# Performance work log

Hardware: AMD Instinct MI355X
Metric: run time of the kernel (lower is better)

## Reference

```python
import jax, jax.numpy as jnp
import numpy as np

B, W, E, P, H, NH = 2, 512, 2, 8, 1024, 16
D = H // NH  # 64
T = W + E


def _split_heads(x):
    # [..., S, H] -> [..., NH, S, D]
    x = x.reshape(x.shape[:-1] + (NH, D))
    return jnp.swapaxes(x, -2, -3)


def setup_inputs() -> dict:
    key = jax.random.key(0)
    ks = jax.random.split(key, 16)
    s = 0.02
    inp = {
        "word_hidden_states": jax.random.normal(ks[0], (B, W, H), jnp.float32),
        "entity_hidden_states": jax.random.normal(ks[1], (B, P, E, H), jnp.float32),
        "attention_mask": jnp.zeros((B, 1, 1, T), jnp.float32),
        "q_w": jax.random.normal(ks[2], (H, H), jnp.float32) * s,
        "q_b": jnp.zeros((H,), jnp.float32),
        "k_w": jax.random.normal(ks[3], (H, H), jnp.float32) * s,
        "k_b": jnp.zeros((H,), jnp.float32),
        "v_w": jax.random.normal(ks[4], (H, H), jnp.float32) * s,
        "v_b": jnp.zeros((H,), jnp.float32),
        "w2e_w": jax.random.normal(ks[5], (H, H), jnp.float32) * s,
        "w2e_b": jnp.zeros((H,), jnp.float32),
        "e2w_w": jax.random.normal(ks[6], (H, H), jnp.float32) * s,
        "e2w_b": jnp.zeros((H,), jnp.float32),
        "e2e_w": jax.random.normal(ks[7], (H, H), jnp.float32) * s,
        "e2e_b": jnp.zeros((H,), jnp.float32),
    }
    return inp


def reference(word_hidden_states, entity_hidden_states, attention_mask,
              q_w, q_b, k_w, k_b, v_w, v_b,
              w2e_w, w2e_b, e2w_w, e2w_b, e2e_w, e2e_b):
    words = word_hidden_states          # [B, W, H]
    ents = entity_hidden_states         # [B, P, E, H]

    # Queries: words use `query` and `w2e_query`; entities use `e2w_query` and `e2e_query`.
    w2w_q = _split_heads(words @ q_w + q_b)      # [B, NH, W, D]
    w2e_q = _split_heads(words @ w2e_w + w2e_b)  # [B, NH, W, D]
    e2w_q = _split_heads(ents @ e2w_w + e2w_b)   # [B, P, NH, E, D]
    e2e_q = _split_heads(ents @ e2e_w + e2e_b)   # [B, P, NH, E, D]

    # Shared key/value projection on [expanded words ; entities]. Word K/V are
    # identical across pairs (expand), so compute once and broadcast.
    k_word = _split_heads(words @ k_w + k_b)     # [B, NH, W, D]
    k_ent = _split_heads(ents @ k_w + k_b)       # [B, P, NH, E, D]
    v_word = _split_heads(words @ v_w + v_b)     # [B, NH, W, D]
    v_ent = _split_heads(ents @ v_w + v_b)       # [B, P, NH, E, D]

    # Four block score matrices.
    s_w2w = jnp.einsum('bhqd,bhkd->bhqk', w2w_q, k_word)      # [B, NH, W, W]
    s_w2e = jnp.einsum('bhqd,bphkd->bphqk', w2e_q, k_ent)     # [B, P, NH, W, E]
    s_e2w = jnp.einsum('bphqd,bhkd->bphqk', e2w_q, k_word)    # [B, P, NH, E, W]
    s_e2e = jnp.einsum('bphqd,bphkd->bphqk', e2e_q, k_ent)    # [B, P, NH, E, E]

    word_scores = jnp.concatenate(
        [jnp.broadcast_to(s_w2w[:, None], (B, P, NH, W, W)), s_w2e], axis=-1)
    ent_scores = jnp.concatenate([s_e2w, s_e2e], axis=-1)
    scores = jnp.concatenate([word_scores, ent_scores], axis=-2)  # [B, P, NH, T, T]

    scale = jnp.asarray(1.0 / np.sqrt(D), scores.dtype)
    scores = scores * scale + attention_mask[:, None]  # mask broadcasts [B,1,1,1,T]
    probs = jax.nn.softmax(scores, axis=-1)  # dropout: eval mode (deterministic)

    v = jnp.concatenate(
        [jnp.broadcast_to(v_word[:, None], (B, P, NH, W, D)), v_ent], axis=-2)
    ctx = jnp.einsum('bphqk,bphkd->bphqd', probs, v)   # [B, P, NH, T, D]
    ctx = jnp.swapaxes(ctx, -2, -3).reshape(B, P, T, H)

    word_reps = ctx[:, :, :W, :]   # [B, P, W, H]
    ent_reps = ctx[:, :, W:, :]    # [B, P, E, H]
    return (word_reps, ent_reps)
```

## Files before the change

kernel.cpp:

```cpp
#include <hip/hip_runtime.h>
#include <hip/hip_bf16.h>

typedef __attribute__((ext_vector_type(8))) short s16x8;
typedef __attribute__((ext_vector_type(4))) float fx4;
typedef __attribute__((ext_vector_type(4))) unsigned int u32x4;
typedef unsigned short u16;
typedef unsigned int   u32;
typedef unsigned long long u64;

#define DI __device__ __forceinline__


DI float bf2f(u16 x){ u32 u = ((u32)x)<<16; float f; __builtin_memcpy(&f,&u,4); return f; }
DI u16 f2bf(float f){ u32 u; __builtin_memcpy(&u,&f,4); u = (u + 0x7fffu + ((u>>16)&1u))>>16; return (u16)u; }

DI fx4 mfma_16x16x32_bf16(s16x8 a, s16x8 b, fx4 c){
  return __builtin_amdgcn_mfma_f32_16x16x32_bf16(a,b,c,0,0,0);
}

__global__ __launch_bounds__(256) void k_prep(
    const float* __restrict__ s0, const float* __restrict__ s1, const float* __restrict__ s2,
    const float* __restrict__ s3, const float* __restrict__ s4, const float* __restrict__ s5,
    u16* __restrict__ dstbase,
    const float* __restrict__ words, u16* __restrict__ Xbf,
    const float* __restrict__ ents,  u16* __restrict__ Ebf)
{
  __shared__ __align__(16) u16 tile[64][72];
  int bx = blockIdx.x, tid = threadIdx.x;
  if(bx < 1536){
    int z = bx>>8, t = bx&255;
    const float* src = (z==0)?s0:(z==1)?s1:(z==2)?s2:(z==3)?s3:(z==4)?s4:s5;
    u16* dst = dstbase + (u64)z*1048576u;
    int kt = (t&15)*64, nt = (t>>4)*64;
    #pragma unroll
    for(int it=0; it<2; ++it){
      int c = it*256 + tid;
      int r = c>>3, col = (c&7)*8;
      const float* sp = src + (u64)(kt+r)*1024u + nt + col;
      fx4 a = *(const fx4*)sp;
      fx4 b = *(const fx4*)(sp+4);
      u16 o[8];
      o[0]=f2bf(a[0]); o[1]=f2bf(a[1]); o[2]=f2bf(a[2]); o[3]=f2bf(a[3]);
      o[4]=f2bf(b[0]); o[5]=f2bf(b[1]); o[6]=f2bf(b[2]); o[7]=f2bf(b[3]);
      __builtin_memcpy(&tile[r][col], o, 16);
    }
    __syncthreads();
    #pragma unroll
    for(int it=0; it<2; ++it){
      int c = it*256 + tid;
      int nr = c>>3, kc = (c&7)*8;
      u16 tmp[8];
      #pragma unroll
      for(int j=0;j<8;++j) tmp[j] = tile[kc+j][nr];
      u32x4 v; __builtin_memcpy(&v, tmp, 16);
      *(u32x4*)(dst + (u64)(nt+nr)*1024u + kt + kc) = v;
    }
  } else {
    const float* src; u16* dst; int i;
    if(bx < 2048){ src = words; dst = Xbf; i = ((bx-1536)*256 + tid)*8; }
    else         { src = ents;  dst = Ebf; i = ((bx-2048)*256 + tid)*8; }
    fx4 a = *(const fx4*)(src+i);
    fx4 b = *(const fx4*)(src+i+4);
    u16 o[8];
    o[0]=f2bf(a[0]); o[1]=f2bf(a[1]); o[2]=f2bf(a[2]); o[3]=f2bf(a[3]);
    o[4]=f2bf(b[0]); o[5]=f2bf(b[1]); o[6]=f2bf(b[2]); o[7]=f2bf(b[3]);
    u32x4 v; __builtin_memcpy(&v,o,16);
    *(u32x4*)(dst+i)=v;
  }
}

__global__ __launch_bounds__(256) void k_proj(
    const u16* __restrict__ Xbf, const u16* __restrict__ Ebf,
    const u16* __restrict__ wtq, const u16* __restrict__ wtw2e,
    const u16* __restrict__ wtk, const u16* __restrict__ wtv,
    const u16* __restrict__ wte2w, const u16* __restrict__ wte2e,
    const float* __restrict__ qb, const float* __restrict__ w2eb,
    const float* __restrict__ kb, const float* __restrict__ vb,
    const float* __restrict__ e2wb, const float* __restrict__ e2eb,
    u16* __restrict__ Qw, u16* __restrict__ Q2e, u16* __restrict__ Kwp, u16* __restrict__ VwTp,
    u16* __restrict__ Qe2w, u16* __restrict__ Qe2e, u16* __restrict__ Kep, u16* __restrict__ VeTp)
{
  __shared__ __align__(16) u16 XL[128*64];
  __shared__ __align__(16) u16 WL[128*64];
  int tid = threadIdx.x;
  int z = blockIdx.z;
  int wv = tid>>6, lane = tid&63, l15 = lane&15, g = lane>>4;

  if(blockIdx.y < 8){
    const u16* WT  = (z==0)?wtq:(z==1)?wtw2e:(z==2)?wtk:wtv;
    const float* bias = (z==0)?qb :(z==1)?w2eb :(z==2)?kb :vb;
    u16* out       = (z==0)?Qw :(z==1)?Q2e :(z==2)?Kwp :VwTp;
    int nt = blockIdx.x*64;
    int mt = blockIdx.y*128;
    int wr = (wv>>1)*64, wc = (wv&1)*32;
    fx4 acc[4][2] = {};
    u32x4 rx[4], rw[2];
    #pragma unroll
    for(int it=0; it<4; ++it){
      int c = it*256 + tid;
      int r = c>>3, cb = (c&7)*16, scb = cb ^ ((r&7)<<4);
      rx[it] = *(const u32x4*)((const char*)Xbf + ((u64)(mt+r)*1024u)*2u + scb);
    }
    #pragma unroll
    for(int it=0; it<2; ++it){
      int c = it*256 + tid;
      int r = c>>3, cb = (c&7)*16, scb = cb ^ ((r&7)<<4);
      rw[it] = *(const u32x4*)((const char*)WT + ((u64)(nt+r)*1024u)*2u + scb);
    }
    #pragma unroll
    for(int it=0; it<4; ++it) *(u32x4*)((char*)XL + (it*256+tid)*16) = rx[it];
    #pragma unroll
    for(int it=0; it<2; ++it) *(u32x4*)((char*)WL + (it*256+tid)*16) = rw[it];
    __syncthreads();
    for(int t=0; t<16; ++t){
      int kn = (t+1)*64;
      if(t < 15){
        #pragma unroll
        for(int it=0; it<4; ++it){
          int c = it*256 + tid;
          int r = c>>3, cb = (c&7)*16, scb = cb ^ ((r&7)<<4);
          rx[it] = *(const u32x4*)((const char*)Xbf + ((u64)(mt+r)*1024u + kn)*2u + scb);
        }
        #pragma unroll
        for(int it=0; it<2; ++it){
          int c = it*256 + tid;
          int r = c>>3, cb = (c&7)*16, scb = cb ^ ((r&7)<<4);
          rw[it] = *(const u32x4*)((const char*)WT + ((u64)(nt+r)*1024u + kn)*2u + scb);
        }
      }
      #pragma unroll
      for(int ks=0; ks<2; ++ks){
        s16x8 af[4], bfv[2];
        #pragma unroll
        for(int i=0;i<4;++i){
          int ra = wr + i*16 + l15;
          af[i]  = *(const s16x8*)((const char*)XL + ra*128 + ((ks*64 + g*16) ^ ((ra&7)<<4)));
        }
        #pragma unroll
        for(int j=0;j<2;++j){
          int rb = wc + j*16 + l15;
          bfv[j] = *(const s16x8*)((const char*)WL + rb*128 + ((ks*64 + g*16) ^ ((rb&7)<<4)));
        }
        #pragma unroll
        for(int i=0;i<4;++i)
          #pragma unroll
          for(int j=0;j<2;++j)
            acc[i][j] = mfma_16x16x32_bf16(af[i], bfv[j], acc[i][j]);
      }
      __syncthreads();
      if(t < 15){
        #pragma unroll
        for(int it=0; it<4; ++it) *(u32x4*)((char*)XL + (it*256+tid)*16) = rx[it];
        #pragma unroll
        for(int it=0; it<2; ++it) *(u32x4*)((char*)WL + (it*256+tid)*16) = rw[it];
        __syncthreads();
      }
    }
    bool vmode = (z==3);
    #pragma unroll
    for(int j=0;j<2;++j){
      int n = nt + wc + j*16 + l15;
      float bv = bias[n];
      int h = n>>6, d = n&63;
      #pragma unroll
      for(int i=0;i<4;++i){
        #pragma unroll
        for(int q=0;q<4;++q){
          int m = mt + wr + i*16 + g*4 + q;
          int bb = m>>9, wrow = m&511;
          float v = acc[i][j][q] + bv;
          u64 o = vmode ? (((u64)(bb*16+h)*64u + d)*512u + wrow)
                        : (((u64)(bb*16+h)*512u + wrow)*64u + d);
          out[o] = f2bf(v);
        }
      }
    }
  } else {
    if(blockIdx.x >= 8) return;
    const u16* WT  = (z==0)?wte2w:(z==1)?wte2e:(z==2)?wtk:wtv;
    const float* bias = (z==0)?e2wb :(z==1)?e2eb :(z==2)?kb :vb;
    u16* out       = (z==0)?Qe2w :(z==1)?Qe2e :(z==2)?Kep :VeTp;
    int nt = blockIdx.x*128;
    int wc = wv*32;
    fx4 acc[2][2] = {};
    for(int kk=0; kk<1024; kk+=64){
      {
        int r = tid>>3, cb = (tid&7)*16, scb = cb ^ ((r&7)<<4);
        *(u32x4*)((char*)XL + r*128 + cb) =
          *(const u32x4*)((const char*)Ebf + ((u64)r*1024u + kk)*2u + scb);
      }
      #pragma unroll
      for(int it=0; it<4; ++it){
        int c = it*256 + tid;
        int r = c>>3, cb = (c&7)*16, scb = cb ^ ((r&7)<<4);
        *(u32x4*)((char*)WL + r*128 + cb) =
          *(const u32x4*)((const char*)WT + ((u64)(nt+r)*1024u + kk)*2u + scb);
      }
      __syncthreads();
      #pragma unroll
      for(int ks=0; ks<2; ++ks){
        s16x8 af[2], bfv[2];
        #pragma unroll
        for(int i=0;i<2;++i){
          int ra = i*16 + l15;
          af[i]  = *(const s16x8*)((const char*)XL + ra*128 + ((ks*64 + g*16) ^ ((ra&7)<<4)));
          int rb = wc + i*16 + l15;
          bfv[i] = *(const s16x8*)((const char*)WL + rb*128 + ((ks*64 + g*16) ^ ((rb&7)<<4)));
        }
        #pragma unroll
        for(int i=0;i<2;++i)
          #pragma unroll
          for(int j=0;j<2;++j)
            acc[i][j] = mfma_16x16x32_bf16(af[i], bfv[j], acc[i][j]);
      }
      __syncthreads();
    }
    bool vmode = (z==3);
    #pragma unroll
    for(int j=0;j<2;++j){
      int n = nt + wc + j*16 + l15;
      float bv = bias[n];
      int h = n>>6, d = n&63;
      #pragma unroll
      for(int i=0;i<2;++i){
        #pragma unroll
        for(int q=0;q<4;++q){
          int m = i*16 + g*4 + q;
          int bb = m>>4, p = (m>>1)&7, e = m&1;
          float v = acc[i][j][q] + bv;
          u64 base = ((u64)(bb*8+p)*16u + h);
          u64 o = vmode ? ((base*64u + d)*2u + e)
                        : ((base*2u + e)*64u + d);
          out[o] = f2bf(v);
        }
      }
    }
  }
}

__global__ __launch_bounds__(256) void k_attn(
    const u16* __restrict__ Qw,  const u16* __restrict__ Q2e,
    const u16* __restrict__ Kw,  const u16* __restrict__ VwT,
    const u16* __restrict__ Ke,  const u16* __restrict__ VeT,
    const u16* __restrict__ Qe2w, const u16* __restrict__ Qe2e,
    const float* __restrict__ msk, float* __restrict__ outw, float* __restrict__ oute)
{
  const float scale = 0.125f;
  __shared__ __align__(16) u16 KL[128*64];
  __shared__ __align__(16) u16 VtL[64*128];
  __shared__ __align__(16) char UA[4][4352];
  __shared__ __align__(16) float mask_lds[576];
  __shared__ __align__(16) float se_lds[4][16][20];
  __shared__ __align__(16) u16 velds[8*128];
  __shared__ float s_lds[2][516];
  __shared__ float qwl[2][64];
  __shared__ float qel[2][64];
  __shared__ float red[2][8];
  int tid = threadIdx.x;
  int h = blockIdx.y, b = blockIdx.z;
  int wv = tid>>6, lane = tid&63, l15 = lane&15, g = lane>>4;

  if(blockIdx.x < 8){
    int qc = blockIdx.x;
    int q0 = qc*64 + wv*16;

    for(int i=tid;i<576;i+=256) mask_lds[i] = (i<514) ? msk[b*514+i] : 0.f;
    if(tid < 128){
      int p = tid>>4, o = (tid&15)*8;
      *(u32x4*)&velds[p*128 + o] = *(const u32x4*)(VeT + ((u64)(b*8+p)*16u + h)*128u + o);
    }

    const u16* Qrow = Qw + ((u64)(b*16+h)*512u + q0 + l15)*64u;
    s16x8 qf0 = *(const s16x8*)(Qrow + g*8);
    s16x8 qf1 = *(const s16x8*)(Qrow + 32 + g*8);
    const u16* Q2row = Q2e + ((u64)(b*16+h)*512u + q0 + l15)*64u;
    s16x8 q2f0 = *(const s16x8*)(Q2row + g*8);
    s16x8 q2f1 = *(const s16x8*)(Q2row + 32 + g*8);
    const u16* kerow = Ke + ((u64)(b*8+(l15>>1))*16u + h)*128u + (u64)(l15&1)*64u;
    s16x8 keA0 = *(const s16x8*)(kerow + g*8);
    s16x8 keA1 = *(const s16x8*)(kerow + 32 + g*8);
    {
      fx4 se = {0.f,0.f,0.f,0.f};
      se = mfma_16x16x32_bf16(keA0, q2f0, se);
      se = mfma_16x16x32_bf16(keA1, q2f1, se);
      *(fx4*)&se_lds[wv][l15][g*4] = se;
    }

    const char* Kpan = (const char*)(Kw  + (u64)(b*16+h)*512u*64u);
    const char* Vpan = (const char*)(VwT + (u64)(b*16+h)*64u*512u);

    u32x4 rk[4], rv[4];
    auto LOADC = [&](int c){
      #pragma unroll
      for(int it=0;it<4;++it){
        int idx = it*256+tid;
        int r = idx>>3, cb = (idx&7)*16;
        rk[it] = *(const u32x4*)(Kpan + (u64)(c*128+r)*128u + cb);
        int vrr = idx>>4, vcb = (idx&15)*16;
        rv[it] = *(const u32x4*)(Vpan + (u64)vrr*1024u + (u64)c*256u + vcb);
      }
    };
    auto WRITEC = [&](){
      #pragma unroll
      for(int it=0;it<4;++it){
        int idx = it*256+tid;
        int r = idx>>3, cb = (idx&7)*16;
        *(u32x4*)((char*)KL + r*128 + (cb ^ ((r&7)<<4))) = rk[it];
        int vrr = idx>>4, vcb = (idx&15)*16;
        *(u32x4*)((char*)VtL + vrr*256 + (vcb ^ ((vrr&15)<<4))) = rv[it];
      }
    };

    LOADC(0); WRITEC();
    float m_run = -3.0e38f, l_run = 0.f;
    fx4 oacc[4] = {};
    __syncthreads();

    char* prow = UA[wv] + l15*272;
    int swzP = (l15&7)<<4;
    for(int c=0;c<4;++c){
      if(c < 3) LOADC(c+1);
      float sv[8][4];
      #pragma unroll
      for(int s=0;s<8;++s){
        int row = s*16 + l15;
        const char* kr = (const char*)KL + row*128;
        int sz = (row&7)<<4;
        s16x8 ka0 = *(const s16x8*)(kr + ((g*16) ^ sz));
        s16x8 ka1 = *(const s16x8*)(kr + ((64 + g*16) ^ sz));
        fx4 st = {0.f,0.f,0.f,0.f};
        st = mfma_16x16x32_bf16(ka0, qf0, st);
        st = mfma_16x16x32_bf16(ka1, qf1, st);
        fx4 mk = *(const fx4*)&mask_lds[c*128 + s*16 + g*4];
        #pragma unroll
        for(int q=0;q<4;++q) sv[s][q] = st[q]*scale + mk[q];
      }
      float cm = -3.0e38f;
      #pragma unroll
      for(int s=0;s<8;++s)
        #pragma unroll
        for(int q=0;q<4;++q) cm = fmaxf(cm, sv[s][q]);
      cm = fmaxf(cm, __shfl_xor(cm, 16, 64));
      cm = fmaxf(cm, __shfl_xor(cm, 32, 64));
      float m_new = fmaxf(m_run, cm);
      float alpha = __expf(m_run - m_new);
      float rs = 0.f;
      #pragma unroll
      for(int s=0;s<8;++s){
        u16 pb4[4];
        #pragma unroll
        for(int q=0;q<4;++q){
          float e = __expf(sv[s][q] - m_new);
          rs += e;
          pb4[q] = f2bf(e);
        }
        u64 packed; __builtin_memcpy(&packed, pb4, 8);
        *(u64*)(prow + ((s*32 + g*8) ^ swzP)) = packed;
      }
      rs += __shfl_xor(rs, 16, 64);
      rs += __shfl_xor(rs, 32, 64);
      l_run = l_run*alpha + rs;
      m_run = m_new;
      #pragma unroll
      for(int t=0;t<4;++t) oacc[t] *= alpha;
      asm volatile("s_waitcnt lgkmcnt(0)" ::: "memory");
      #pragma unroll
      for(int kh=0;kh<4;++kh){
        s16x8 pbig = *(const s16x8*)(prow + ((kh*64 + g*16) ^ swzP));
        #pragma unroll
        for(int t=0;t<4;++t){
          int vrow = t*16 + l15;
          const char* vr = (const char*)VtL + vrow*256 + ((kh*64 + g*16) ^ ((vrow&15)<<4));
          s16x8 va = *(const s16x8*)vr;
          oacc[t] = mfma_16x16x32_bf16(va, pbig, oacc[t]);
        }
      }
      __syncthreads();
      if(c < 3){ WRITEC(); __syncthreads(); }
    }

    #pragma unroll
    for(int t=0;t<4;++t){
      fx4 w = oacc[t];
      *(fx4*)(prow + ((t*64 + g*16) ^ swzP)) = w;
    }
    asm volatile("s_waitcnt lgkmcnt(0)" ::: "memory");

    int r = lane>>2, cbo = (lane&3)*16;
    const char* orow = UA[wv] + r*272;
    int swzR = (r&7)<<4;
    fx4 N0 = *(const fx4*)(orow + (((lane&3)*64 +  0) ^ swzR));
    fx4 N1 = *(const fx4*)(orow + (((lane&3)*64 + 16) ^ swzR));
    fx4 N2 = *(const fx4*)(orow + (((lane&3)*64 + 32) ^ swzR));
    fx4 N3 = *(const fx4*)(orow + (((lane&3)*64 + 48) ^ swzR));
    float m_r = __shfl(m_run, r, 64);
    float l_r = __shfl(l_run, r, 64);
    float mke0 = mask_lds[512], mke1 = mask_lds[513];

    for(int p=0;p<8;++p){
      float s0 = se_lds[wv][r][2*p]  *scale + mke0;
      float s1 = se_lds[wv][r][2*p+1]*scale + mke1;
      float mp = fmaxf(m_r, fmaxf(s0, s1));
      float al = __expf(m_r - mp);
      float p0 = __expf(s0-mp), p1 = __expf(s1-mp);
      float linv = 1.0f/(l_r*al + p0 + p1);
      const u16* vep = velds + p*128 + cbo*2;
      u16 ve[32];
      {
        u32x4 w0 = *(const u32x4*)vep;
        u32x4 w1 = *(const u32x4*)(vep+8);
        u32x4 w2 = *(const u32x4*)(vep+16);
        u32x4 w3 = *(const u32x4*)(vep+24);
        __builtin_memcpy(ve,    &w0, 16);
        __builtin_memcpy(ve+8,  &w1, 16);
        __builtin_memcpy(ve+16, &w2, 16);
        __builtin_memcpy(ve+24, &w3, 16);
      }
      float o[16];
      #pragma unroll
      for(int j=0;j<4;++j){
        o[j]    = (N0[j]*al + p0*bf2f(ve[2*j])      + p1*bf2f(ve[2*j+1]))*linv;
        o[4+j]  = (N1[j]*al + p0*bf2f(ve[8+2*j])    + p1*bf2f(ve[8+2*j+1]))*linv;
        o[8+j]  = (N2[j]*al + p0*bf2f(ve[16+2*j])   + p1*bf2f(ve[16+2*j+1]))*linv;
        o[12+j] = (N3[j]*al + p0*bf2f(ve[24+2*j])   + p1*bf2f(ve[24+2*j+1]))*linv;
      }
      float* og = outw + ((u64)(b*8+p)*512u + q0 + r)*1024u + h*64 + cbo;
      *(fx4*)og      = *(const fx4*)&o[0];
      *(fx4*)(og+4)  = *(const fx4*)&o[4];
      *(fx4*)(og+8)  = *(const fx4*)&o[8];
      *(fx4*)(og+12) = *(const fx4*)&o[12];
    }
  } else {
    int p = blockIdx.x - 8;
    u64 ebase = (u64)(b*8+p)*16u + h;
    if(tid < 128){
      int r = tid>>6, d = tid&63;
      qwl[r][d] = bf2f(Qe2w[(ebase*2 + r)*64 + d]);
      qel[r][d] = bf2f(Qe2e[(ebase*2 + r)*64 + d]);
    }
    __syncthreads();
    const u16* Kpan = Kw + (u64)(b*16+h)*512u*64u;
    for(int k=tid;k<512;k+=256){
      const u16* kr = Kpan + (u64)k*64u;
      float d0=0.f, d1=0.f;
      #pragma unroll
      for(int j=0;j<64;j+=8){
        s16x8 kv = *(const s16x8*)(kr+j);
        #pragma unroll
        for(int x=0;x<8;++x){
          float kf = bf2f((u16)kv[x]);
          d0 += qwl[0][j+x]*kf;
          d1 += qwl[1][j+x]*kf;
        }
      }
      float mk = msk[b*514 + k];
      s_lds[0][k] = d0*0.125f + mk;
      s_lds[1][k] = d1*0.125f + mk;
    }
    if(tid < 4){
      int r = tid>>1, e = tid&1;
      const u16* kr = Ke + (ebase*2 + e)*64;
      float dd = 0.f;
      for(int j=0;j<64;++j) dd += qel[r][j]*bf2f(kr[j]);
      s_lds[r][512+e] = dd*0.125f + msk[b*514 + 512 + e];
    }
    __syncthreads();
    float mx0=-3e38f, mx1=-3e38f;
    for(int k=tid;k<514;k+=256){ mx0=fmaxf(mx0,s_lds[0][k]); mx1=fmaxf(mx1,s_lds[1][k]); }
    #pragma unroll
    for(int off=32; off; off>>=1){
      mx0 = fmaxf(mx0, __shfl_xor(mx0, off, 64));
      mx1 = fmaxf(mx1, __shfl_xor(mx1, off, 64));
    }
    if(lane==0){ red[0][wv]=mx0; red[1][wv]=mx1; }
    __syncthreads();
    float m0 = fmaxf(fmaxf(red[0][0],red[0][1]),fmaxf(red[0][2],red[0][3]));
    float m1 = fmaxf(fmaxf(red[1][0],red[1][1]),fmaxf(red[1][2],red[1][3]));
    float sm0=0.f, sm1=0.f;
    for(int k=tid;k<514;k+=256){
      float e0 = __expf(s_lds[0][k]-m0); s_lds[0][k]=e0; sm0+=e0;
      float e1 = __expf(s_lds[1][k]-m1); s_lds[1][k]=e1; sm1+=e1;
    }
    #pragma unroll
    for(int off=32; off; off>>=1){
      sm0 += __shfl_xor(sm0, off, 64);
      sm1 += __shfl_xor(sm1, off, 64);
    }
    if(lane==0){ red[0][4+wv]=sm0; red[1][4+wv]=sm1; }
    __syncthreads();
    float l0 = red[0][4]+red[0][5]+red[0][6]+red[0][7];
    float l1 = red[1][4]+red[1][5]+red[1][6]+red[1][7];
    if(tid < 128){
      int r = tid>>6, d = tid&63;
      const u16* vr = VwT + ((u64)(b*16+h)*64u + d)*512u;
      float acc = 0.f;
      for(int k=0;k<512;k+=8){
        s16x8 vv = *(const s16x8*)(vr+k);
        #pragma unroll
        for(int x=0;x<8;++x) acc += s_lds[r][k+x]*bf2f((u16)vv[x]);
      }
      const u16* ve = VeT + (ebase*64 + d)*2;
      acc += s_lds[r][512]*bf2f(ve[0]) + s_lds[r][513]*bf2f(ve[1]);
      float val = acc / ((r==0)?l0:l1);
      oute[(((u64)(b*8+p)*2u + r)*1024u + h*64 + d)] = val;
    }
  }
}

extern "C" void kernel_launch(void* const* d_in, const int* in_sizes, int n_in,
                              void* d_out, int out_size, void* d_ws, size_t ws_size,
                              hipStream_t stream)
{
  const float* words = (const float*)d_in[0];
  const float* ents  = (const float*)d_in[1];
  const float* amask = (const float*)d_in[2];
  const float* q_w   = (const float*)d_in[3];
  const float* q_b   = (const float*)d_in[4];
  const float* k_w   = (const float*)d_in[5];
  const float* k_b   = (const float*)d_in[6];
  const float* v_w   = (const float*)d_in[7];
  const float* v_b   = (const float*)d_in[8];
  const float* w2e_w = (const float*)d_in[9];
  const float* w2e_b = (const float*)d_in[10];
  const float* e2w_w = (const float*)d_in[11];
  const float* e2w_b = (const float*)d_in[12];
  const float* e2e_w = (const float*)d_in[13];
  const float* e2e_b = (const float*)d_in[14];

  const size_t MW = 1048576;
  u16* ws16 = (u16*)d_ws;
  if(ws_size < (11*MW + 5*32768)*sizeof(u16)) return;
  u16* WTq   = ws16 + 0*MW;
  u16* WTk   = ws16 + 1*MW;
  u16* WTv   = ws16 + 2*MW;
  u16* WTw2e = ws16 + 3*MW;
  u16* WTe2w = ws16 + 4*MW;
  u16* WTe2e = ws16 + 5*MW;
  u16* Qw    = ws16 + 6*MW;
  u16* Q2e   = ws16 + 7*MW;
  u16* Kwp   = ws16 + 8*MW;
  u16* VwTp  = ws16 + 9*MW;
  u16* Xbf   = ws16 + 10*MW;
  u16* Qe2w  = ws16 + 11*MW;
  u16* Qe2e  = Qe2w + 32768;
  u16* Kep   = Qe2e + 32768;
  u16* VeTp  = Kep + 32768;
  u16* Ebf   = VeTp + 32768;

  dim3 tb(256);
  k_prep<<<dim3(2064), tb, 0, stream>>>(q_w, k_w, v_w, w2e_w, e2w_w, e2e_w, ws16,
                                        words, Xbf, ents, Ebf);
  k_proj<<<dim3(16,9,4), tb, 0, stream>>>(Xbf, Ebf,
      WTq, WTw2e, WTk, WTv, WTe2w, WTe2e,
      q_b, w2e_b, k_b, v_b, e2w_b, e2e_b,
      Qw, Q2e, Kwp, VwTp, Qe2w, Qe2e, Kep, VeTp);
  k_attn<<<dim3(16,16,2), tb, 0, stream>>>(Qw, Q2e, Kwp, VwTp, Kep, VeTp,
      Qe2w, Qe2e, amask, (float*)d_out, (float*)d_out + 8388608u);
}
```

Before: 63.31 us.

## Halve query rows per attention block, shrink LDS, and double word-query grid

Word-query attention blocks now cover 32 queries (8 per wave) instead of 64, so there are twice as many of them (grid x grows from 16 to 24). The MFMA tiles run with duplicated query rows, and only half the lanes store output. LDS use drops: the score-exchange buffer is replaced by register shuffles, the entity V staging buffer becomes direct global reads, and the entity-branch scratch reuses the K tile buffer. The goal is better occupancy and more blocks across CUs, at the cost of wasted MFMA work and K/V panel reloads for every query chunk.

Result: slower. 68.82 us (+8.7%).

```diff
diff --git a/kernel.cpp b/kernel.cpp
--- a/kernel.cpp
+++ b/kernel.cpp
@@ -248,43 +248,31 @@
   const float scale = 0.125f;
   __shared__ __align__(16) u16 KL[128*64];
   __shared__ __align__(16) u16 VtL[64*128];
-  __shared__ __align__(16) char UA[4][4352];
-  __shared__ __align__(16) float mask_lds[576];
-  __shared__ __align__(16) float se_lds[4][16][20];
-  __shared__ __align__(16) u16 velds[8*128];
-  __shared__ float s_lds[2][516];
-  __shared__ float qwl[2][64];
-  __shared__ float qel[2][64];
-  __shared__ float red[2][8];
+  __shared__ __align__(16) char UA[4][4096];
+  __shared__ __align__(16) float mask_lds[516];
   int tid = threadIdx.x;
   int h = blockIdx.y, b = blockIdx.z;
   int wv = tid>>6, lane = tid&63, l15 = lane&15, g = lane>>4;
 
-  if(blockIdx.x < 8){
+  if(blockIdx.x < 16){
     int qc = blockIdx.x;
-    int q0 = qc*64 + wv*16;
-
-    for(int i=tid;i<576;i+=256) mask_lds[i] = (i<514) ? msk[b*514+i] : 0.f;
-    if(tid < 128){
-      int p = tid>>4, o = (tid&15)*8;
-      *(u32x4*)&velds[p*128 + o] = *(const u32x4*)(VeT + ((u64)(b*8+p)*16u + h)*128u + o);
-    }
-
-    const u16* Qrow = Qw + ((u64)(b*16+h)*512u + q0 + l15)*64u;
+    int q0 = qc*32 + wv*8;
+
+    for(int i=tid;i<516;i+=256) mask_lds[i] = (i<514) ? msk[b*514+i] : 0.f;
+
+    int qrow = q0 + (l15&7);
+    const u16* Qrow = Qw + ((u64)(b*16+h)*512u + qrow)*64u;
     s16x8 qf0 = *(const s16x8*)(Qrow + g*8);
     s16x8 qf1 = *(const s16x8*)(Qrow + 32 + g*8);
-    const u16* Q2row = Q2e + ((u64)(b*16+h)*512u + q0 + l15)*64u;
+    const u16* Q2row = Q2e + ((u64)(b*16+h)*512u + qrow)*64u;
     s16x8 q2f0 = *(const s16x8*)(Q2row + g*8);
     s16x8 q2f1 = *(const s16x8*)(Q2row + 32 + g*8);
     const u16* kerow = Ke + ((u64)(b*8+(l15>>1))*16u + h)*128u + (u64)(l15&1)*64u;
     s16x8 keA0 = *(const s16x8*)(kerow + g*8);
     s16x8 keA1 = *(const s16x8*)(kerow + 32 + g*8);
-    {
-      fx4 se = {0.f,0.f,0.f,0.f};
-      se = mfma_16x16x32_bf16(keA0, q2f0, se);
-      se = mfma_16x16x32_bf16(keA1, q2f1, se);
-      *(fx4*)&se_lds[wv][l15][g*4] = se;
-    }
+    fx4 se = {0.f,0.f,0.f,0.f};
+    se = mfma_16x16x32_bf16(keA0, q2f0, se);
+    se = mfma_16x16x32_bf16(keA1, q2f1, se);
 
     const char* Kpan = (const char*)(Kw  + (u64)(b*16+h)*512u*64u);
     const char* Vpan = (const char*)(VwT + (u64)(b*16+h)*64u*512u);
@@ -316,8 +304,8 @@
     fx4 oacc[4] = {};
     __syncthreads();
 
-    char* prow = UA[wv] + l15*272;
-    int swzP = (l15&7)<<4;
+    char* prow = UA[wv] + l15*256;
+    int swzP = (l15&15)<<4;
     for(int c=0;c<4;++c){
       if(c < 3) LOADC(c+1);
       float sv[8][4];
@@ -387,8 +375,8 @@
     asm volatile("s_waitcnt lgkmcnt(0)" ::: "memory");
 
     int r = lane>>2, cbo = (lane&3)*16;
-    const char* orow = UA[wv] + r*272;
-    int swzR = (r&7)<<4;
+    const char* orow = UA[wv] + r*256;
+    int swzR = (r&15)<<4;
     fx4 N0 = *(const fx4*)(orow + (((lane&3)*64 +  0) ^ swzR));
     fx4 N1 = *(const fx4*)(orow + (((lane&3)*64 + 16) ^ swzR));
     fx4 N2 = *(const fx4*)(orow + (((lane&3)*64 + 32) ^ swzR));
@@ -396,15 +384,18 @@
     float m_r = __shfl(m_run, r, 64);
     float l_r = __shfl(l_run, r, 64);
     float mke0 = mask_lds[512], mke1 = mask_lds[513];
-
+    bool valid = (r < 8);
+
+    #pragma unroll
     for(int p=0;p<8;++p){
-      float s0 = se_lds[wv][r][2*p]  *scale + mke0;
-      float s1 = se_lds[wv][r][2*p+1]*scale + mke1;
+      int srcl = (p>>1)*16 + r;
+      float s0 = __shfl(se[(2*p)&3],   srcl, 64)*scale + mke0;
+      float s1 = __shfl(se[(2*p+1)&3], srcl, 64)*scale + mke1;
       float mp = fmaxf(m_r, fmaxf(s0, s1));
       float al = __expf(m_r - mp);
       float p0 = __expf(s0-mp), p1 = __expf(s1-mp);
       float linv = 1.0f/(l_r*al + p0 + p1);
-      const u16* vep = velds + p*128 + cbo*2;
+      const u16* vep = VeT + ((u64)(b*8+p)*16u + h)*128u + cbo*2;
       u16 ve[32];
       {
         u32x4 w0 = *(const u32x4*)vep;
@@ -424,19 +415,26 @@
         o[8+j]  = (N2[j]*al + p0*bf2f(ve[16+2*j])   + p1*bf2f(ve[16+2*j+1]))*linv;
         o[12+j] = (N3[j]*al + p0*bf2f(ve[24+2*j])   + p1*bf2f(ve[24+2*j+1]))*linv;
       }
-      float* og = outw + ((u64)(b*8+p)*512u + q0 + r)*1024u + h*64 + cbo;
-      *(fx4*)og      = *(const fx4*)&o[0];
-      *(fx4*)(og+4)  = *(const fx4*)&o[4];
-      *(fx4*)(og+8)  = *(const fx4*)&o[8];
-      *(fx4*)(og+12) = *(const fx4*)&o[12];
+      if(valid){
+        float* og = outw + ((u64)(b*8+p)*512u + q0 + r)*1024u + h*64 + cbo;
+        *(fx4*)og      = *(const fx4*)&o[0];
+        *(fx4*)(og+4)  = *(const fx4*)&o[4];
+        *(fx4*)(og+8)  = *(const fx4*)&o[8];
+        *(fx4*)(og+12) = *(const fx4*)&o[12];
+      }
     }
   } else {
-    int p = blockIdx.x - 8;
+    int p = blockIdx.x - 16;
     u64 ebase = (u64)(b*8+p)*16u + h;
+    float* s0_ = (float*)KL;
+    float* s1_ = s0_ + 516;
+    float* qwl = (float*)((char*)KL + 4160);
+    float* qel = qwl + 128;
+    float* red_ = qel + 128;
     if(tid < 128){
       int r = tid>>6, d = tid&63;
-      qwl[r][d] = bf2f(Qe2w[(ebase*2 + r)*64 + d]);
-      qel[r][d] = bf2f(Qe2e[(ebase*2 + r)*64 + d]);
+      qwl[r*64+d] = bf2f(Qe2w[(ebase*2 + r)*64 + d]);
+      qel[r*64+d] = bf2f(Qe2e[(ebase*2 + r)*64 + d]);
     }
     __syncthreads();
     const u16* Kpan = Kw + (u64)(b*16+h)*512u*64u;
@@ -449,58 +447,60 @@
         #pragma unroll
         for(int x=0;x<8;++x){
           float kf = bf2f((u16)kv[x]);
-          d0 += qwl[0][j+x]*kf;
-          d1 += qwl[1][j+x]*kf;
+          d0 += qwl[j+x]*kf;
+          d1 += qwl[64+j+x]*kf;
         }
       }
       float mk = msk[b*514 + k];
-      s_lds[0][k] = d0*0.125f + mk;
-      s_lds[1][k] = d1*0.125f + mk;
+      s0_[k] = d0*0.125f + mk;
+      s1_[k] = d1*0.125f + mk;
     }
     if(tid < 4){
       int r = tid>>1, e = tid&1;
       const u16* kr = Ke + (ebase*2 + e)*64;
       float dd = 0.f;
-      for(int j=0;j<64;++j) dd += qel[r][j]*bf2f(kr[j]);
-      s_lds[r][512+e] = dd*0.125f + msk[b*514 + 512 + e];
+      for(int j=0;j<64;++j) dd += qel[r*64+j]*bf2f(kr[j]);
+      float* sl = (r==0)?s0_:s1_;
+      sl[512+e] = dd*0.125f + msk[b*514 + 512 + e];
     }
     __syncthreads();
     float mx0=-3e38f, mx1=-3e38f;
-    for(int k=tid;k<514;k+=256){ mx0=fmaxf(mx0,s_lds[0][k]); mx1=fmaxf(mx1,s_lds[1][k]); }
+    for(int k=tid;k<514;k+=256){ mx0=fmaxf(mx0,s0_[k]); mx1=fmaxf(mx1,s1_[k]); }
     #pragma unroll
     for(int off=32; off; off>>=1){
       mx0 = fmaxf(mx0, __shfl_xor(mx0, off, 64));
       mx1 = fmaxf(mx1, __shfl_xor(mx1, off, 64));
     }
-    if(lane==0){ red[0][wv]=mx0; red[1][wv]=mx1; }
-    __syncthreads();
-    float m0 = fmaxf(fmaxf(red[0][0],red[0][1]),fmaxf(red[0][2],red[0][3]));
-    float m1 = fmaxf(fmaxf(red[1][0],red[1][1]),fmaxf(red[1][2],red[1][3]));
+    if(lane==0){ red_[wv]=mx0; red_[8+wv]=mx1; }
+    __syncthreads();
+    float m0 = fmaxf(fmaxf(red_[0],red_[1]),fmaxf(red_[2],red_[3]));
+    float m1 = fmaxf(fmaxf(red_[8],red_[9]),fmaxf(red_[10],red_[11]));
     float sm0=0.f, sm1=0.f;
     for(int k=tid;k<514;k+=256){
-      float e0 = __expf(s_lds[0][k]-m0); s_lds[0][k]=e0; sm0+=e0;
-      float e1 = __expf(s_lds[1][k]-m1); s_lds[1][k]=e1; sm1+=e1;
+      float e0 = __expf(s0_[k]-m0); s0_[k]=e0; sm0+=e0;
+      float e1 = __expf(s1_[k]-m1); s1_[k]=e1; sm1+=e1;
     }
     #pragma unroll
     for(int off=32; off; off>>=1){
       sm0 += __shfl_xor(sm0, off, 64);
       sm1 += __shfl_xor(sm1, off, 64);
     }
-    if(lane==0){ red[0][4+wv]=sm0; red[1][4+wv]=sm1; }
-    __syncthreads();
-    float l0 = red[0][4]+red[0][5]+red[0][6]+red[0][7];
-    float l1 = red[1][4]+red[1][5]+red[1][6]+red[1][7];
+    if(lane==0){ red_[4+wv]=sm0; red_[12+wv]=sm1; }
+    __syncthreads();
+    float l0 = red_[4]+red_[5]+red_[6]+red_[7];
+    float l1 = red_[12]+red_[13]+red_[14]+red_[15];
     if(tid < 128){
       int r = tid>>6, d = tid&63;
+      const float* sl = (r==0)?s0_:s1_;
       const u16* vr = VwT + ((u64)(b*16+h)*64u + d)*512u;
       float acc = 0.f;
       for(int k=0;k<512;k+=8){
         s16x8 vv = *(const s16x8*)(vr+k);
         #pragma unroll
-        for(int x=0;x<8;++x) acc += s_lds[r][k+x]*bf2f((u16)vv[x]);
+        for(int x=0;x<8;++x) acc += sl[k+x]*bf2f((u16)vv[x]);
       }
       const u16* ve = VeT + (ebase*64 + d)*2;
-      acc += s_lds[r][512]*bf2f(ve[0]) + s_lds[r][513]*bf2f(ve[1]);
+      acc += sl[512]*bf2f(ve[0]) + sl[513]*bf2f(ve[1]);
       float val = acc / ((r==0)?l0:l1);
       oute[(((u64)(b*8+p)*2u + r)*1024u + h*64 + d)] = val;
     }
@@ -554,6 +554,6 @@
       WTq, WTw2e, WTk, WTv, WTe2w, WTe2e,
       q_b, w2e_b, k_b, v_b, e2w_b, e2e_b,
       Qw, Q2e, Kwp, VwTp, Qe2w, Qe2e, Kep, VeTp);
-  k_attn<<<dim3(16,16,2), tb, 0, stream>>>(Qw, Q2e, Kwp, VwTp, Kep, VeTp,
+  k_attn<<<dim3(24,16,2), tb, 0, stream>>>(Qw, Q2e, Kwp, VwTp, Kep, VeTp,
       Qe2w, Qe2e, amask, (float*)d_out, (float*)d_out + 8388608u);
 }
```
